# Kernel optimization log

Measured on AMD Instinct MI355X. Metric: run time of the kernel, lower is better.

## Reference

```python
import jax, jax.numpy as jnp
import numpy as np

N = 100000   # nodes
E = 1000000  # edges
IN, H, OUT = 256, 64, 16


def setup_inputs() -> dict:
    key = jax.random.key(0)
    k0, k1, k2, k3 = jax.random.split(key, 4)
    x = jax.random.normal(k0, (N, IN), jnp.float32)
    edge_index = jax.random.randint(k1, (2, E), 0, N)
    # GCNConv parameters (glorot-ish weights, zero bias as in PyG defaults)
    W1 = jax.random.normal(k2, (IN, H), jnp.float32) / np.sqrt(IN).astype(np.float32)
    b1 = jnp.zeros((H,), jnp.float32)
    W2 = jax.random.normal(k3, (H, OUT), jnp.float32) / np.sqrt(H).astype(np.float32)
    b2 = jnp.zeros((OUT,), jnp.float32)
    return {"x": x, "edge_index": edge_index, "W1": W1, "b1": b1, "W2": W2, "b2": b2}


def gcn_conv(x, W, b, src, dst, n):
    # PyG GCNConv: h = x @ W; out[v] = sum_{(u->v)} norm(u,v) * h[u] + b
    h = x @ W                                    # [n, out]
    deg = jnp.zeros((n,), h.dtype).at[dst].add(1.0)
    dinv = jnp.where(deg > 0, jax.lax.rsqrt(deg), 0.0)
    norm = dinv[src] * dinv[dst]                 # [E+n] symmetric normalization
    msg = h[src] * norm[:, None]                 # gather + scale
    agg = jax.ops.segment_sum(msg, dst, num_segments=n)  # scatter-add
    return agg + b


def reference(x, edge_index, W1, b1, W2, b2):
    n = x.shape[0]
    # add self-loops (PyG GCNConv default add_self_loops=True)
    loops = jnp.arange(n, dtype=edge_index.dtype)
    src = jnp.concatenate([edge_index[0], loops])
    dst = jnp.concatenate([edge_index[1], loops])
    h = gcn_conv(x, W1, b1, src, dst, n)
    h = jax.nn.relu(h)  # F.dropout is identity in eval mode (training=False)
    return gcn_conv(h, W2, b2, src, dst, n)
```

## Files before the change

### kernel.cpp

```cpp
#include <hip/hip_runtime.h>

namespace {
constexpr int NN  = 100000;
constexpr int NE  = 1000000;
constexpr int INF = 256;
constexpr int HF  = 64;
constexpr int OF  = 16;
constexpr int SCAN_CHUNK = 1024;
constexpr int NBLK = (NN + SCAN_CHUNK - 1) / SCAN_CHUNK;
constexpr int NSEG = 8;
constexpr int SEGW = (NN + NSEG - 1) / NSEG;
constexpr int CNTW = 100096;
constexpr int ZBLK = (CNTW / 4 + 255) / 256;
}

typedef __attribute__((ext_vector_type(8))) short     sh8;
typedef __attribute__((ext_vector_type(4))) float     f32x4;
typedef __attribute__((ext_vector_type(8))) unsigned short us8;

__device__ __forceinline__ unsigned short f2bf(float f) {
    unsigned int u = __builtin_bit_cast(unsigned int, f);
    u += 0x7FFFu + ((u >> 16) & 1u);
    return (unsigned short)(u >> 16);
}
__device__ __forceinline__ float bf2f(unsigned short s) {
    return __builtin_bit_cast(float, (unsigned int)s << 16);
}

__global__ void k_pre(int* __restrict__ cnt, const float* __restrict__ W1,
                      unsigned short* __restrict__ wt_g) {
    int b = blockIdx.x, t = threadIdx.x;
    if (b < ZBLK) {
        int i = (b * 256 + t) * 4;
        if (i < CNTW) *(int4*)(cnt + i) = (int4){0, 0, 0, 0};
    } else {
        int idx = (b - ZBLK) * 256 + t;
        int c = idx >> 8, k = idx & 255;
        wt_g[idx] = f2bf(W1[(size_t)k * HF + c]);
    }
}

__global__ void k_hist(const int* __restrict__ dst, int* __restrict__ cnt) {
    int b     = blockIdx.x;
    int seg   = b & (NSEG - 1);
    int chunk = b >> 3;
    int e = chunk * 256 + threadIdx.x;
    if (e < NE) {
        int d = dst[e];
        if ((unsigned)d / (unsigned)SEGW == (unsigned)seg)
            atomicAdd(&cnt[d], 1);
    }
}

__global__ __launch_bounds__(256) void k_reduce(const int* __restrict__ cnt,
                                                int* __restrict__ bsum,
                                                float* __restrict__ dinv) {
    int t = threadIdx.x;
    int i0 = blockIdx.x * SCAN_CHUNK + t * 4;
    int s = 0;
    float dv[4] = {0.f, 0.f, 0.f, 0.f};
    #pragma unroll
    for (int q = 0; q < 4; ++q) {
        if (i0 + q < NN) {
            int c = cnt[i0 + q];
            s += c;
            dv[q] = rsqrtf((float)(c + 1));
        }
    }
    if (i0 + 3 < NN) *(float4*)(dinv + i0) = (float4){dv[0], dv[1], dv[2], dv[3]};
    else { for (int q = 0; q < 4; ++q) if (i0 + q < NN) dinv[i0 + q] = dv[q]; }
    #pragma unroll
    for (int off = 32; off > 0; off >>= 1) s += __shfl_down(s, off);
    __shared__ int wsum[4];
    int lane = t & 63, wid = t >> 6;
    if (lane == 0) wsum[wid] = s;
    __syncthreads();
    if (t == 0) bsum[blockIdx.x] = wsum[0] + wsum[1] + wsum[2] + wsum[3];
}

__global__ void k_partials(int* __restrict__ bsum) {
    int l = threadIdx.x;
    int a0 = (l < NBLK) ? bsum[l] : 0;
    int b0 = (64 + l < NBLK) ? bsum[64 + l] : 0;
    int a = a0, b = b0;
    #pragma unroll
    for (int off = 1; off < 64; off <<= 1) {
        int na = __shfl_up(a, off); if (l >= off) a += na;
        int nb = __shfl_up(b, off); if (l >= off) b += nb;
    }
    int tot = __shfl(a, 63);
    if (l < NBLK) bsum[l] = a - a0;
    if (64 + l < NBLK) bsum[64 + l] = tot + b - b0;
}

__global__ __launch_bounds__(256) void k_scan(const int* __restrict__ cnt,
                                              const int* __restrict__ bsum,
                                              int* __restrict__ rowptr,
                                              int* __restrict__ cursor) {
    int t = threadIdx.x;
    int i0 = blockIdx.x * SCAN_CHUNK + t * 4;
    int v0 = 0, v1 = 0, v2 = 0, v3 = 0;
    if (i0 + 0 < NN) v0 = cnt[i0 + 0];
    if (i0 + 1 < NN) v1 = cnt[i0 + 1];
    if (i0 + 2 < NN) v2 = cnt[i0 + 2];
    if (i0 + 3 < NN) v3 = cnt[i0 + 3];
    int tsum = v0 + v1 + v2 + v3;
    int lane = t & 63, wid = t >> 6;
    int incl = tsum;
    #pragma unroll
    for (int off = 1; off < 64; off <<= 1) {
        int n = __shfl_up(incl, off);
        if (lane >= off) incl += n;
    }
    __shared__ int wsum[4];
    if (lane == 63) wsum[wid] = incl;
    __syncthreads();
    int woff = 0;
    for (int w = 0; w < wid; ++w) woff += wsum[w];
    int excl = woff + (incl - tsum) + bsum[blockIdx.x];
    int e0 = excl, e1 = e0 + v0, e2 = e1 + v1, e3 = e2 + v2;
    if (i0 + 0 < NN) { rowptr[i0 + 0] = e0; cursor[i0 + 0] = e0; }
    if (i0 + 1 < NN) { rowptr[i0 + 1] = e1; cursor[i0 + 1] = e1; }
    if (i0 + 2 < NN) { rowptr[i0 + 2] = e2; cursor[i0 + 2] = e2; }
    if (i0 + 3 < NN) { rowptr[i0 + 3] = e3; cursor[i0 + 3] = e3; }
    if (i0 + 3 == NN - 1) rowptr[NN] = e3 + v3;
}

__global__ __launch_bounds__(256) void k_scatter(const int* __restrict__ src,
                                                 const int* __restrict__ dst,
                                                 int* __restrict__ cursor,
                                                 int* __restrict__ eidx) {
    int b     = blockIdx.x;
    int seg   = b & (NSEG - 1);
    int chunk = b >> 3;
    int e = chunk * 256 + threadIdx.x;
    if (e < NE) {
        int d = dst[e];
        if ((unsigned)d / (unsigned)SEGW == (unsigned)seg) {
            int p = atomicAdd(&cursor[d], 1);
            eidx[p] = src[e];
        }
    }
}

__global__ __launch_bounds__(256, 4) void k_gemm1(const float* __restrict__ x,
                                                  const unsigned short* __restrict__ wt_g,
                                                  unsigned short* __restrict__ h1) {
    __shared__ unsigned short wt[64 * 264];
    int t = threadIdx.x;
    int w = t >> 6, l = t & 63;
    int row0 = blockIdx.x * 128;

    #pragma unroll
    for (int p = 0; p < 8; ++p) {
        int T   = p * 256 + t;
        int c   = T >> 5;
        int kb8 = T & 31;
        *(us8*)(wt + c * 264 + kb8 * 8) = *(const us8*)(wt_g + c * 256 + kb8 * 8);
    }
    __syncthreads();

    int m = l & 15;
    int g = l >> 4;
    int gr0 = row0 + w * 32 + m;      if (gr0 > NN - 1) gr0 = NN - 1;
    int gr1 = row0 + w * 32 + 16 + m; if (gr1 > NN - 1) gr1 = NN - 1;
    const float* p0 = x + (size_t)gr0 * INF + g * 8;
    const float* p1 = x + (size_t)gr1 * INF + g * 8;

    f32x4 acc[2][4];
    #pragma unroll
    for (int i = 0; i < 2; ++i)
        #pragma unroll
        for (int j = 0; j < 4; ++j) acc[i][j] = (f32x4){0.f, 0.f, 0.f, 0.f};

    #pragma unroll 2
    for (int kb = 0; kb < INF; kb += 32) {
        float4 u0 = *(const float4*)(p0 + kb);
        float4 u1 = *(const float4*)(p0 + kb + 4);
        float4 u2 = *(const float4*)(p1 + kb);
        float4 u3 = *(const float4*)(p1 + kb + 4);
        us8 a0u = { f2bf(u0.x), f2bf(u0.y), f2bf(u0.z), f2bf(u0.w),
                    f2bf(u1.x), f2bf(u1.y), f2bf(u1.z), f2bf(u1.w) };
        us8 a1u = { f2bf(u2.x), f2bf(u2.y), f2bf(u2.z), f2bf(u2.w),
                    f2bf(u3.x), f2bf(u3.y), f2bf(u3.z), f2bf(u3.w) };
        sh8 a0 = __builtin_bit_cast(sh8, a0u);
        sh8 a1 = __builtin_bit_cast(sh8, a1u);
        #pragma unroll
        for (int nt = 0; nt < 4; ++nt) {
            sh8 b = *(const sh8*)(wt + (nt * 16 + m) * 264 + kb + g * 8);
            acc[0][nt] = __builtin_amdgcn_mfma_f32_16x16x32_bf16(a0, b, acc[0][nt], 0, 0, 0);
            acc[1][nt] = __builtin_amdgcn_mfma_f32_16x16x32_bf16(a1, b, acc[1][nt], 0, 0, 0);
        }
    }

    #pragma unroll
    for (int mt = 0; mt < 2; ++mt) {
        #pragma unroll
        for (int r = 0; r < 4; ++r) {
            int gr = row0 + w * 32 + mt * 16 + (l >> 4) * 4 + r;
            if (gr < NN) {
                #pragma unroll
                for (int nt = 0; nt < 4; ++nt)
                    h1[(size_t)gr * HF + nt * 16 + (l & 15)] = f2bf(acc[mt][nt][r]);
            }
        }
    }
}

__global__ __launch_bounds__(256) void k_gather1(const int* __restrict__ rowptr,
                                                 const int* __restrict__ eidx,
                                                 const float* __restrict__ dinv,
                                                 const unsigned short* __restrict__ h1,
                                                 const float* __restrict__ b1,
                                                 const float* __restrict__ W2,
                                                 float* __restrict__ h2) {
    __shared__ float w2L[HF * OF];
    __shared__ float hrL[32][HF + 4];
    int t = threadIdx.x;
    *(float4*)(w2L + t * 4) = *(const float4*)(W2 + t * 4);

    int nodeL = t >> 3;
    int fg    = t & 7;
    int v     = blockIdx.x * 32 + nodeL;
    int beg = rowptr[v], end = rowptr[v + 1];

    float acc[8] = {};
    for (int i = beg; i < end; ++i) {
        int s = eidx[i];
        float wgt = dinv[s];
        us8 hv = *(const us8*)(h1 + (size_t)s * HF + fg * 8);
        #pragma unroll
        for (int q = 0; q < 8; ++q) acc[q] += wgt * bf2f(hv[q]);
    }

    {
        float dv = dinv[v], sl = dv * dv;
        us8 hv = *(const us8*)(h1 + (size_t)v * HF + fg * 8);
        #pragma unroll
        for (int q = 0; q < 8; ++q) {
            float val = dv * acc[q] + sl * bf2f(hv[q]) + b1[fg * 8 + q];
            hrL[nodeL][fg * 8 + q] = val > 0.f ? val : 0.f;
        }
    }
    __syncthreads();

    #pragma unroll
    for (int T = t; T < 512; T += 256) {
        int n = T >> 4, j = T & 15;
        const float* hr = hrL[n];
        float p = 0.f;
        #pragma unroll
        for (int k = 0; k < HF; ++k) p += hr[k] * w2L[k * OF + j];
        h2[(size_t)(blockIdx.x * 32 + n) * OF + j] = p;
    }
}

__global__ __launch_bounds__(256) void k_gather2(const int* __restrict__ rowptr,
                                                 const int* __restrict__ eidx,
                                                 const float* __restrict__ dinv,
                                                 const float* __restrict__ h2,
                                                 const float* __restrict__ b2,
                                                 float* __restrict__ out) {
    int gid   = blockIdx.x * 256 + threadIdx.x;
    int v     = gid >> 6;
    int lane  = threadIdx.x & 63;
    int eslot = lane >> 2;
    int fg    = lane & 3;
    int beg = rowptr[v], end = rowptr[v + 1];
    float4 acc = {0.f, 0.f, 0.f, 0.f};
    for (int i = beg + eslot; i < end; i += 16) {
        int s = eidx[i];
        float w = dinv[s];
        float4 hv = *(const float4*)(h2 + (size_t)s * OF + fg * 4);
        acc.x += w * hv.x; acc.y += w * hv.y; acc.z += w * hv.z; acc.w += w * hv.w;
    }
    #pragma unroll
    for (int m = 4; m <= 32; m <<= 1) {
        acc.x += __shfl_xor(acc.x, m);
        acc.y += __shfl_xor(acc.y, m);
        acc.z += __shfl_xor(acc.z, m);
        acc.w += __shfl_xor(acc.w, m);
    }
    if (eslot == 0) {
        float dv = dinv[v];
        float sl = dv * dv;
        float4 hv = *(const float4*)(h2 + (size_t)v * OF + fg * 4);
        float4 bv = *(const float4*)(b2 + fg * 4);
        float4 o;
        o.x = dv * acc.x + sl * hv.x + bv.x;
        o.y = dv * acc.y + sl * hv.y + bv.y;
        o.z = dv * acc.z + sl * hv.z + bv.z;
        o.w = dv * acc.w + sl * hv.w + bv.w;
        *(float4*)(out + (size_t)v * OF + fg * 4) = o;
    }
}

extern "C" void kernel_launch(void* const* d_in, const int* in_sizes, int n_in,
                              void* d_out, int out_size, void* d_ws, size_t ws_size,
                              hipStream_t stream) {
    const float* x   = (const float*)d_in[0];
    const int*   ei  = (const int*)d_in[1];
    const int*   src = ei;
    const int*   dst = ei + NE;
    const float* W1  = (const float*)d_in[2];
    const float* b1  = (const float*)d_in[3];
    const float* W2  = (const float*)d_in[4];
    const float* b2  = (const float*)d_in[5];
    float* out = (float*)d_out;

    float* dinv  = (float*)d_ws;
    unsigned short* h1b = (unsigned short*)(dinv + CNTW);
    float* h2    = (float*)(h1b + (size_t)NN * HF);
    int*   cnt   = (int*)(h2 + (size_t)NN * OF);
    int*   rowptr = cnt + CNTW;
    int*   cursor = rowptr + 100352;
    int*   eidx  = cursor + CNTW;
    int*   bsum  = eidx + NE;
    unsigned short* wt_g = (unsigned short*)(bsum + 128);

    k_pre<<<ZBLK + 64, 256, 0, stream>>>(cnt, W1, wt_g);
    k_hist<<<((NE + 255) / 256) * NSEG, 256, 0, stream>>>(dst, cnt);
    k_reduce<<<NBLK, 256, 0, stream>>>(cnt, bsum, dinv);
    k_partials<<<1, 64, 0, stream>>>(bsum);
    k_scan<<<NBLK, 256, 0, stream>>>(cnt, bsum, rowptr, cursor);
    k_scatter<<<((NE + 255) / 256) * NSEG, 256, 0, stream>>>(src, dst, cursor, eidx);

    k_gemm1<<<(NN + 127) / 128, 256, 0, stream>>>(x, wt_g, h1b);
    k_gather1<<<NN / 32, 256, 0, stream>>>(rowptr, eidx, dinv, h1b, b1, W2, h2);

    k_gather2<<<(NN * HF) / 256, 256, 0, stream>>>(rowptr, eidx, dinv, h2, b2, out);
}
```

Before: 188.5 us.

## Fold block-prefix into scan, store h2 as bf16, prefetch gathers, remap gather2

Removes the single-block partials kernel by having each scan block sum the preceding block totals itself with a wave reduction. Stores the layer-2 projection h2 in bf16 instead of fp32, which halves gather traffic in the second aggregation at some precision cost. Adds one-step software prefetching of the next neighbor index, weight and features in both gather loops. Remaps gather2 so that 16 lanes per node each own one output feature and walk the whole edge list sequentially, instead of 16 edge slots per node combined with a cross-lane shuffle reduction.

```diff
diff --git a/kernel.cpp b/kernel.cpp
--- a/kernel.cpp
+++ b/kernel.cpp
@@ -78,34 +78,28 @@
     if (t == 0) bsum[blockIdx.x] = wsum[0] + wsum[1] + wsum[2] + wsum[3];
 }
 
-__global__ void k_partials(int* __restrict__ bsum) {
-    int l = threadIdx.x;
-    int a0 = (l < NBLK) ? bsum[l] : 0;
-    int b0 = (64 + l < NBLK) ? bsum[64 + l] : 0;
-    int a = a0, b = b0;
-    #pragma unroll
-    for (int off = 1; off < 64; off <<= 1) {
-        int na = __shfl_up(a, off); if (l >= off) a += na;
-        int nb = __shfl_up(b, off); if (l >= off) b += nb;
-    }
-    int tot = __shfl(a, 63);
-    if (l < NBLK) bsum[l] = a - a0;
-    if (64 + l < NBLK) bsum[64 + l] = tot + b - b0;
-}
-
 __global__ __launch_bounds__(256) void k_scan(const int* __restrict__ cnt,
                                               const int* __restrict__ bsum,
                                               int* __restrict__ rowptr,
                                               int* __restrict__ cursor) {
     int t = threadIdx.x;
-    int i0 = blockIdx.x * SCAN_CHUNK + t * 4;
+    int b = blockIdx.x;
+    int lane = t & 63, wid = t >> 6;
+
+    int p = 0;
+    if (lane < b) p += bsum[lane];
+    if (64 + lane < b) p += bsum[64 + lane];
+    #pragma unroll
+    for (int off = 32; off > 0; off >>= 1) p += __shfl_down(p, off);
+    int blockBase = __shfl(p, 0);
+
+    int i0 = b * SCAN_CHUNK + t * 4;
     int v0 = 0, v1 = 0, v2 = 0, v3 = 0;
     if (i0 + 0 < NN) v0 = cnt[i0 + 0];
     if (i0 + 1 < NN) v1 = cnt[i0 + 1];
     if (i0 + 2 < NN) v2 = cnt[i0 + 2];
     if (i0 + 3 < NN) v3 = cnt[i0 + 3];
     int tsum = v0 + v1 + v2 + v3;
-    int lane = t & 63, wid = t >> 6;
     int incl = tsum;
     #pragma unroll
     for (int off = 1; off < 64; off <<= 1) {
@@ -117,7 +111,7 @@
     __syncthreads();
     int woff = 0;
     for (int w = 0; w < wid; ++w) woff += wsum[w];
-    int excl = woff + (incl - tsum) + bsum[blockIdx.x];
+    int excl = woff + (incl - tsum) + blockBase;
     int e0 = excl, e1 = e0 + v0, e2 = e1 + v1, e3 = e2 + v2;
     if (i0 + 0 < NN) { rowptr[i0 + 0] = e0; cursor[i0 + 0] = e0; }
     if (i0 + 1 < NN) { rowptr[i0 + 1] = e1; cursor[i0 + 1] = e1; }
@@ -213,7 +207,7 @@
                                                  const unsigned short* __restrict__ h1,
                                                  const float* __restrict__ b1,
                                                  const float* __restrict__ W2,
-                                                 float* __restrict__ h2) {
+                                                 unsigned short* __restrict__ h2) {
     __shared__ float w2L[HF * OF];
     __shared__ float hrL[32][HF + 4];
     int t = threadIdx.x;
@@ -225,12 +219,21 @@
     int beg = rowptr[v], end = rowptr[v + 1];
 
     float acc[8] = {};
+    int   s_n = 0;  float w_n = 0.f;  us8 h_n = {};
+    if (beg < end) {
+        s_n = eidx[beg];
+        w_n = dinv[s_n];
+        h_n = *(const us8*)(h1 + (size_t)s_n * HF + fg * 8);
+    }
     for (int i = beg; i < end; ++i) {
-        int s = eidx[i];
-        float wgt = dinv[s];
-        us8 hv = *(const us8*)(h1 + (size_t)s * HF + fg * 8);
-        #pragma unroll
-        for (int q = 0; q < 8; ++q) acc[q] += wgt * bf2f(hv[q]);
+        float w_c = w_n;  us8 h_c = h_n;
+        if (i + 1 < end) {
+            s_n = eidx[i + 1];
+            w_n = dinv[s_n];
+            h_n = *(const us8*)(h1 + (size_t)s_n * HF + fg * 8);
+        }
+        #pragma unroll
+        for (int q = 0; q < 8; ++q) acc[q] += w_c * bf2f(h_c[q]);
     }
 
     {
@@ -251,48 +254,40 @@
         float p = 0.f;
         #pragma unroll
         for (int k = 0; k < HF; ++k) p += hr[k] * w2L[k * OF + j];
-        h2[(size_t)(blockIdx.x * 32 + n) * OF + j] = p;
+        h2[(size_t)(blockIdx.x * 32 + n) * OF + j] = f2bf(p);
     }
 }
 
 __global__ __launch_bounds__(256) void k_gather2(const int* __restrict__ rowptr,
                                                  const int* __restrict__ eidx,
                                                  const float* __restrict__ dinv,
-                                                 const float* __restrict__ h2,
+                                                 const unsigned short* __restrict__ h2,
                                                  const float* __restrict__ b2,
                                                  float* __restrict__ out) {
-    int gid   = blockIdx.x * 256 + threadIdx.x;
-    int v     = gid >> 6;
-    int lane  = threadIdx.x & 63;
-    int eslot = lane >> 2;
-    int fg    = lane & 3;
+    int t     = threadIdx.x;
+    int nodeL = t >> 4;
+    int j     = t & 15;
+    int v     = blockIdx.x * 16 + nodeL;
     int beg = rowptr[v], end = rowptr[v + 1];
-    float4 acc = {0.f, 0.f, 0.f, 0.f};
-    for (int i = beg + eslot; i < end; i += 16) {
-        int s = eidx[i];
-        float w = dinv[s];
-        float4 hv = *(const float4*)(h2 + (size_t)s * OF + fg * 4);
-        acc.x += w * hv.x; acc.y += w * hv.y; acc.z += w * hv.z; acc.w += w * hv.w;
-    }
-    #pragma unroll
-    for (int m = 4; m <= 32; m <<= 1) {
-        acc.x += __shfl_xor(acc.x, m);
-        acc.y += __shfl_xor(acc.y, m);
-        acc.z += __shfl_xor(acc.z, m);
-        acc.w += __shfl_xor(acc.w, m);
-    }
-    if (eslot == 0) {
-        float dv = dinv[v];
-        float sl = dv * dv;
-        float4 hv = *(const float4*)(h2 + (size_t)v * OF + fg * 4);
-        float4 bv = *(const float4*)(b2 + fg * 4);
-        float4 o;
-        o.x = dv * acc.x + sl * hv.x + bv.x;
-        o.y = dv * acc.y + sl * hv.y + bv.y;
-        o.z = dv * acc.z + sl * hv.z + bv.z;
-        o.w = dv * acc.w + sl * hv.w + bv.w;
-        *(float4*)(out + (size_t)v * OF + fg * 4) = o;
-    }
+
+    float acc = 0.f;
+    int   s_n = 0;  float w_n = 0.f;  unsigned short h_n = 0;
+    if (beg < end) {
+        s_n = eidx[beg];
+        w_n = dinv[s_n];
+        h_n = h2[(size_t)s_n * OF + j];
+    }
+    for (int i = beg; i < end; ++i) {
+        float w_c = w_n;  unsigned short h_c = h_n;
+        if (i + 1 < end) {
+            s_n = eidx[i + 1];
+            w_n = dinv[s_n];
+            h_n = h2[(size_t)s_n * OF + j];
+        }
+        acc += w_c * bf2f(h_c);
+    }
+    float dv = dinv[v];
+    out[(size_t)v * OF + j] = dv * acc + dv * dv * bf2f(h2[(size_t)v * OF + j]) + b2[j];
 }
 
 extern "C" void kernel_launch(void* const* d_in, const int* in_sizes, int n_in,
@@ -310,8 +305,8 @@
 
     float* dinv  = (float*)d_ws;
     unsigned short* h1b = (unsigned short*)(dinv + CNTW);
-    float* h2    = (float*)(h1b + (size_t)NN * HF);
-    int*   cnt   = (int*)(h2 + (size_t)NN * OF);
+    unsigned short* h2b = (unsigned short*)(h1b + (size_t)NN * HF);
+    int*   cnt   = (int*)(h2b + (size_t)NN * OF + (size_t)NN * OF);
     int*   rowptr = cnt + CNTW;
     int*   cursor = rowptr + 100352;
     int*   eidx  = cursor + CNTW;
@@ -321,12 +316,11 @@
     k_pre<<<ZBLK + 64, 256, 0, stream>>>(cnt, W1, wt_g);
     k_hist<<<((NE + 255) / 256) * NSEG, 256, 0, stream>>>(dst, cnt);
     k_reduce<<<NBLK, 256, 0, stream>>>(cnt, bsum, dinv);
-    k_partials<<<1, 64, 0, stream>>>(bsum);
     k_scan<<<NBLK, 256, 0, stream>>>(cnt, bsum, rowptr, cursor);
     k_scatter<<<((NE + 255) / 256) * NSEG, 256, 0, stream>>>(src, dst, cursor, eidx);
 
     k_gemm1<<<(NN + 127) / 128, 256, 0, stream>>>(x, wt_g, h1b);
-    k_gather1<<<NN / 32, 256, 0, stream>>>(rowptr, eidx, dinv, h1b, b1, W2, h2);
-
-    k_gather2<<<(NN * HF) / 256, 256, 0, stream>>>(rowptr, eidx, dinv, h2, b2, out);
-}
+    k_gather1<<<NN / 32, 256, 0, stream>>>(rowptr, eidx, dinv, h1b, b1, W2, h2b);
+
+    k_gather2<<<NN / 16, 256, 0, stream>>>(rowptr, eidx, dinv, h2b, b2, out);
+}
```

After: 191.2 us. Within noise of the previous version (+1.5%).
